# Kernel tuning notes

Measured on AMD Instinct MI355X. Metric: run time of the kernel, lower is better.

## Reference

```python
import jax, jax.numpy as jnp
import numpy as np

TEMPERATURE = 0.1

# Constant linear map replacing the nested-loop diagonal masks:
# M[i, j, k] = 1 if i + j == k, shape (10, 10, 19).
_ii, _jj = np.meshgrid(np.arange(10), np.arange(10), indexing='ij')
_M = np.zeros((10, 10, 19), dtype=np.float32)
_M[_ii, _jj, _ii + _jj] = 1.0
DIAG_SUM = jnp.asarray(_M)


def setup_inputs() -> dict:
    key = jax.random.key(0)
    ks = jax.random.split(key, 8)
    B = 16384
    grid = jax.random.normal(ks[0], (B, 4, 28, 28), dtype=jnp.float32)
    # random one-hot program ids
    pid = jax.random.randint(ks[1], (B,), 0, 4)
    program_onehot = jax.nn.one_hot(pid, 4, dtype=jnp.float32)
    W1 = jax.random.normal(ks[2], (784, 256), dtype=jnp.float32) * 0.05
    b1 = jnp.zeros((256,), dtype=jnp.float32)
    W2 = jax.random.normal(ks[3], (256, 10), dtype=jnp.float32) * 0.05
    b2 = jnp.zeros((10,), dtype=jnp.float32)
    Wp = jax.random.normal(ks[4], (4, 16), dtype=jnp.float32) * 0.3
    bp = jnp.zeros((16,), dtype=jnp.float32)
    Wr1 = jax.random.normal(ks[5], (16, 4), dtype=jnp.float32) * 0.3
    br1 = jnp.zeros((4,), dtype=jnp.float32)
    Wr2 = jax.random.normal(ks[6], (16, 4), dtype=jnp.float32) * 0.3
    br2 = jnp.zeros((4,), dtype=jnp.float32)
    return {"grid": grid, "program_onehot": program_onehot,
            "W1": W1, "b1": b1, "W2": W2, "b2": b2,
            "Wp": Wp, "bp": bp, "Wr1": Wr1, "br1": br1,
            "Wr2": Wr2, "br2": br2}


def reference(grid, program_onehot, W1, b1, W2, b2, Wp, bp, Wr1, br1, Wr2, br2):
    B = grid.shape[0]
    # digit_net: 784 -> 256 -> 10 MLP on each of the 4 sub-images
    x = grid.reshape(B * 4, 784)
    h1 = jax.nn.relu(x @ W1 + b1)
    logits = h1 @ W2 + b2                       # (B*4, 10)
    digit_probs = jax.nn.softmax(logits / TEMPERATURE, axis=-1).reshape(B, 4, 10)
    # pointer network
    h = program_onehot @ Wp + bp                 # (B, 16)
    ptr1 = jax.nn.softmax(h @ Wr1 + br1, axis=-1)  # (B, 4)
    ptr2 = jax.nn.softmax(h @ Wr2 + br2, axis=-1)  # (B, 4)
    dist1 = jnp.einsum('bp,bpd->bd', ptr1, digit_probs)  # (B, 10)
    dist2 = jnp.einsum('bp,bpd->bd', ptr2, digit_probs)  # (B, 10)
    outer = dist1[:, :, None] * dist2[:, None, :]         # (B, 10, 10)
    outer_sym = 0.5 * (outer + jnp.swapaxes(outer, 1, 2))
    # diagonal-sum convolution as one contraction against the constant map
    sum_distribution = jnp.einsum('bij,ijk->bk', outer_sym, DIAG_SUM)  # (B, 19)
    return jnp.log(sum_distribution + 1e-10)
```

## Files before the change

### kernel.cpp

```cpp
#include <hip/hip_runtime.h>
#include <hip/hip_bf16.h>

typedef __attribute__((ext_vector_type(8))) short bf16x8;
typedef __attribute__((ext_vector_type(4))) float f32x4;

__device__ __forceinline__ short f2bf(float f) {
    union { float f; unsigned u; } v; v.f = f;
    unsigned r = v.u + 0x7fffu + ((v.u >> 16) & 1u);
    return (short)(r >> 16);
}

#define KP  800
#define LDK 40
#define NKT 25

__global__ __launch_bounds__(256) void init_kernel(
    const float* __restrict__ W1, const float* __restrict__ W2,
    const float* __restrict__ Wp, const float* __restrict__ bp,
    const float* __restrict__ Wr1, const float* __restrict__ br1,
    const float* __restrict__ Wr2, const float* __restrict__ br2,
    short* __restrict__ w1t, short* __restrict__ w2t,
    float* __restrict__ ptabs)
{
    const int b = blockIdx.x;
    if (b < 200) {
        const int kt = b >> 3, nt = b & 7;
        __shared__ float tile[32][33];
        const int x = threadIdx.x & 31, y = threadIdx.x >> 5;
        #pragma unroll
        for (int r = 0; r < 4; ++r) {
            int kl = y + r * 8;
            int k = kt * 32 + kl, n = nt * 32 + x;
            tile[kl][x] = (k < 784) ? W1[k * 256 + n] : 0.f;
        }
        __syncthreads();
        #pragma unroll
        for (int r = 0; r < 4; ++r) {
            int nl = y + r * 8;
            int n = nt * 32 + nl, k = kt * 32 + x;
            w1t[n * KP + k] = f2bf(tile[x][nl]);
        }
    } else {
        for (int i = threadIdx.x; i < 16 * 256; i += 256) {
            int n = i >> 8, k = i & 255;
            float v = (n < 10) ? W2[k * 10 + n] : 0.f;
            w2t[i] = f2bf(v);
        }
        if (threadIdx.x < 8) {
            int which = threadIdx.x >> 2, p = threadIdx.x & 3;
            const float* Wr = which ? Wr2 : Wr1;
            const float* br = which ? br2 : br1;
            float s[4];
            for (int q = 0; q < 4; q++) {
                float a = br[q];
                for (int j = 0; j < 16; j++) a += (Wp[p * 16 + j] + bp[j]) * Wr[j * 4 + q];
                s[q] = a;
            }
            float m = fmaxf(fmaxf(s[0], s[1]), fmaxf(s[2], s[3]));
            float e[4]; float tot = 0.f;
            for (int q = 0; q < 4; q++) { e[q] = __expf(s[q] - m); tot += e[q]; }
            for (int q = 0; q < 4; q++) ptabs[which * 16 + p * 4 + q] = e[q] / tot;
        }
    }
}

__global__ __launch_bounds__(512, 4) void fused_kernel(
    const float* __restrict__ g_in, const float* __restrict__ onehot,
    const float* __restrict__ b1g, const float* __restrict__ b2g,
    const short* __restrict__ w1t, const short* __restrict__ w2t,
    const float* __restrict__ ptabs, float* __restrict__ out)
{
    __shared__ __align__(16) char lds[78464];
    short* Abuf = (short*)lds;
    short* Bbuf = (short*)(lds + 20480);
    short* h1   = (short*)lds;
    float* probs = (float*)(lds + 67584);
    float* dist1 = (float*)(lds + 75776);
    float* dist2 = (float*)(lds + 77056);

    const int t = threadIdx.x;
    const int lane = t & 63, wave = t >> 6;
    const int l16 = lane & 15, lg = lane >> 4;
    const int wr = wave >> 2, wc = wave & 3;
    const int blk = blockIdx.x;

    const int ar = t >> 2, aq = t & 3;
    const int bn = t >> 1, bh = t & 1;
    const float* gA = g_in + ((long)blk * 128 + ar) * 784 + aq * 8;
    const short* gB = w1t + bn * KP + bh * 16;
    short* awp = Abuf + ar * LDK + aq * 8;
    short* bwp = Bbuf + bn * LDK + bh * 16;

    f32x4 acc[4][4];
    #pragma unroll
    for (int mi = 0; mi < 4; mi++)
        #pragma unroll
        for (int ni = 0; ni < 4; ni++)
            acc[mi][ni] = (f32x4)0.f;

    f32x4 x0, x1; bf16x8 y0, y1;
    auto load_tile = [&](int kt) {
        const int k0 = kt * 32;
        if (k0 + aq * 8 < 784) {
            x0 = *(const f32x4*)(gA + k0);
            x1 = *(const f32x4*)(gA + k0 + 4);
        } else { x0 = (f32x4)0.f; x1 = (f32x4)0.f; }
        y0 = *(const bf16x8*)(gB + k0);
        y1 = *(const bf16x8*)(gB + k0 + 8);
    };
    auto write_tile = [&](int buf) {
        bf16x8 a8;
        a8[0] = f2bf(x0[0]); a8[1] = f2bf(x0[1]); a8[2] = f2bf(x0[2]); a8[3] = f2bf(x0[3]);
        a8[4] = f2bf(x1[0]); a8[5] = f2bf(x1[1]); a8[6] = f2bf(x1[2]); a8[7] = f2bf(x1[3]);
        *(bf16x8*)(awp + buf * (128 * LDK)) = a8;
        *(bf16x8*)(bwp + buf * (256 * LDK)) = y0;
        *(bf16x8*)(bwp + buf * (256 * LDK) + 8) = y1;
    };

    load_tile(0); write_tile(0);
    __syncthreads();
    int cur = 0;
    for (int kt = 0; kt < NKT; kt++) {
        const bool more = (kt + 1 < NKT);
        if (more) load_tile(kt + 1);
        const short* ab = Abuf + cur * (128 * LDK);
        const short* bb = Bbuf + cur * (256 * LDK);
        bf16x8 aF[4], bF[4];
        #pragma unroll
        for (int mi = 0; mi < 4; mi++)
            aF[mi] = *(const bf16x8*)(ab + (wr * 64 + mi * 16 + l16) * LDK + lg * 8);
        #pragma unroll
        for (int ni = 0; ni < 4; ni++)
            bF[ni] = *(const bf16x8*)(bb + (wc * 64 + ni * 16 + l16) * LDK + lg * 8);
        #pragma unroll
        for (int mi = 0; mi < 4; mi++)
            #pragma unroll
            for (int ni = 0; ni < 4; ni++)
                acc[mi][ni] = __builtin_amdgcn_mfma_f32_16x16x32_bf16(aF[mi], bF[ni], acc[mi][ni], 0, 0, 0);
        if (more) write_tile(cur ^ 1);
        __syncthreads();
        cur ^= 1;
    }

    #pragma unroll
    for (int mi = 0; mi < 4; mi++) {
        const int R = wr * 64 + mi * 16 + lg * 4;
        #pragma unroll
        for (int ni = 0; ni < 4; ni++) {
            const int N = wc * 64 + ni * 16 + l16;
            const float bias = b1g[N];
            #pragma unroll
            for (int j = 0; j < 4; j++) {
                float v = acc[mi][ni][j] + bias;
                h1[(R + j) * 264 + N] = f2bf(fmaxf(v, 0.f));
            }
        }
    }
    __syncthreads();

    f32x4 acc2 = (f32x4)0.f;
    const short* h1r = h1 + (wave * 16 + l16) * 264 + lg * 8;
    const short* w2r = w2t + l16 * 256 + lg * 8;
    #pragma unroll
    for (int kk = 0; kk < 8; kk++) {
        bf16x8 a2 = *(const bf16x8*)(h1r + kk * 32);
        bf16x8 b2f = *(const bf16x8*)(w2r + kk * 32);
        acc2 = __builtin_amdgcn_mfma_f32_16x16x32_bf16(a2, b2f, acc2, 0, 0, 0);
    }

    const float b2v = (l16 < 10) ? b2g[l16] : 0.f;
    float pv[4], mx[4];
    #pragma unroll
    for (int j = 0; j < 4; j++) {
        pv[j] = (l16 < 10) ? (acc2[j] + b2v) * 10.f : -1e30f;
        mx[j] = pv[j];
    }
    #pragma unroll
    for (int off = 1; off < 16; off <<= 1)
        #pragma unroll
        for (int j = 0; j < 4; j++)
            mx[j] = fmaxf(mx[j], __shfl_xor(mx[j], off));
    float ex[4], sm[4];
    #pragma unroll
    for (int j = 0; j < 4; j++) { ex[j] = __expf(pv[j] - mx[j]); sm[j] = ex[j]; }
    #pragma unroll
    for (int off = 1; off < 16; off <<= 1)
        #pragma unroll
        for (int j = 0; j < 4; j++)
            sm[j] += __shfl_xor(sm[j], off);
    #pragma unroll
    for (int j = 0; j < 4; j++)
        probs[(wave * 16 + lg * 4 + j) * 16 + l16] = ex[j] / sm[j];
    __syncthreads();

    if (t < 320) {
        int s = t / 10, d = t - s * 10;
        const float* oh = onehot + ((long)blk * 32 + s) * 4;
        int pid = (int)(oh[1] + 2.f * oh[2] + 3.f * oh[3] + 0.5f);
        const float* p1t = ptabs + pid * 4;
        const float* p2t = ptabs + 16 + pid * 4;
        float d1 = 0.f, d2 = 0.f;
        #pragma unroll
        for (int p = 0; p < 4; p++) {
            float pr = probs[(s * 4 + p) * 16 + d];
            d1 += p1t[p] * pr;
            d2 += p2t[p] * pr;
        }
        dist1[s * 10 + d] = d1;
        dist2[s * 10 + d] = d2;
    }
    __syncthreads();

    for (int idx = t; idx < 608; idx += 512) {
        int s = idx / 19, k = idx - s * 19;
        int ilo = k > 9 ? k - 9 : 0;
        int ihi = k < 9 ? k : 9;
        float sum = 0.f;
        for (int i = ilo; i <= ihi; i++)
            sum += dist1[s * 10 + i] * dist2[s * 10 + (k - i)];
        out[((long)blk * 32 + s) * 19 + k] = __logf(sum + 1e-10f);
    }
}

extern "C" void kernel_launch(void* const* d_in, const int* in_sizes, int n_in,
                              void* d_out, int out_size, void* d_ws, size_t ws_size,
                              hipStream_t stream)
{
    const float* grid   = (const float*)d_in[0];
    const float* onehot = (const float*)d_in[1];
    const float* W1  = (const float*)d_in[2];
    const float* b1  = (const float*)d_in[3];
    const float* W2  = (const float*)d_in[4];
    const float* b2  = (const float*)d_in[5];
    const float* Wp  = (const float*)d_in[6];
    const float* bp  = (const float*)d_in[7];
    const float* Wr1 = (const float*)d_in[8];
    const float* br1 = (const float*)d_in[9];
    const float* Wr2 = (const float*)d_in[10];
    const float* br2 = (const float*)d_in[11];
    float* out = (float*)d_out;

    short* w1t = (short*)d_ws;
    short* w2t = w1t + 256 * KP;
    float* ptabs = (float*)(w2t + 16 * 256);

    init_kernel<<<201, 256, 0, stream>>>(W1, W2, Wp, bp, Wr1, br1, Wr2, br2, w1t, w2t, ptabs);

    const int B = in_sizes[1] / 4;
    const int nblk = (B * 4) / 128;
    fused_kernel<<<nblk, 512, 0, stream>>>(grid, onehot, b1, b2, w1t, w2t, ptabs, out);
}
```

Before: 56.20 us.

## Stream W1 tiles directly to LDS with swizzle and triple-buffered pipeline

Loads the bf16 W1 tiles with global_load_lds straight into a triple-buffered, XOR-swizzled LDS layout instead of staging them through registers, and restructures the K loop into a two-step unrolled pipeline with explicit vmcnt/lgkmcnt waits and raw barriers. This is meant to cut register pressure and VGPR-to-LDS store traffic and to overlap more global loads with MFMA work. It relies on hand-placed waitcnt values and scheduling barriers, so correctness depends on the exact count of in-flight loads.

```diff
diff --git a/kernel.cpp b/kernel.cpp
--- a/kernel.cpp
+++ b/kernel.cpp
@@ -10,9 +10,24 @@
     return (short)(r >> 16);
 }
 
+__device__ __forceinline__ void gl2lds16(const void* g, void* l) {
+    __builtin_amdgcn_global_load_lds(
+        (const __attribute__((address_space(1))) unsigned int*)g,
+        (__attribute__((address_space(3))) unsigned int*)l,
+        16, 0, 0);
+}
+
 #define KP  800
 #define LDK 40
-#define NKT 25
+#define ABS (128 * LDK)
+#define BBS (256 * 32)
+#define BBSB 16384
+
+#define WAITV2 asm volatile("s_waitcnt vmcnt(2)" ::: "memory")
+#define WAITV0 asm volatile("s_waitcnt vmcnt(0)" ::: "memory")
+#define WAITL  asm volatile("s_waitcnt lgkmcnt(0)" ::: "memory")
+#define SBAR   __builtin_amdgcn_s_barrier()
+#define SCHED0 __builtin_amdgcn_sched_barrier(0)
 
 __global__ __launch_bounds__(256) void init_kernel(
     const float* __restrict__ W1, const float* __restrict__ W2,
@@ -70,13 +85,13 @@
     const short* __restrict__ w1t, const short* __restrict__ w2t,
     const float* __restrict__ ptabs, float* __restrict__ out)
 {
-    __shared__ __align__(16) char lds[78464];
+    __shared__ __align__(16) char lds[78336];
     short* Abuf = (short*)lds;
     short* Bbuf = (short*)(lds + 20480);
     short* h1   = (short*)lds;
-    float* probs = (float*)(lds + 67584);
-    float* dist1 = (float*)(lds + 75776);
-    float* dist2 = (float*)(lds + 77056);
+    float* dist1 = (float*)(lds + 67584);
+    float* dist2 = (float*)(lds + 68864);
+    float* probs = (float*)(lds + 70144);
 
     const int t = threadIdx.x;
     const int lane = t & 63, wave = t >> 6;
@@ -85,11 +100,12 @@
     const int blk = blockIdx.x;
 
     const int ar = t >> 2, aq = t & 3;
-    const int bn = t >> 1, bh = t & 1;
     const float* gA = g_in + ((long)blk * 128 + ar) * 784 + aq * 8;
-    const short* gB = w1t + bn * KP + bh * 16;
     short* awp = Abuf + ar * LDK + aq * 8;
-    short* bwp = Bbuf + bn * LDK + bh * 16;
+    const int brow = t >> 2;
+    const short* gBsw = w1t + brow * KP + ((aq ^ (brow & 3)) * 8);
+    char* ldsB = (char*)Bbuf;
+    const int bswz = lg ^ (l16 & 3);
 
     f32x4 acc[4][4];
     #pragma unroll
@@ -98,49 +114,62 @@
         for (int ni = 0; ni < 4; ni++)
             acc[mi][ni] = (f32x4)0.f;
 
-    f32x4 x0, x1; bf16x8 y0, y1;
-    auto load_tile = [&](int kt) {
+    f32x4 xa0, xa1, xb0, xb1;
+
+    auto issueB = [&](int s) {
+        const short* g0 = gBsw + s * 32;
+        char* l0 = ldsB + (s % 3) * BBSB + wave * 1024;
+        gl2lds16(g0, l0);
+        gl2lds16(g0 + 128 * KP, l0 + 8192);
+    };
+    auto issueA = [&](int kt, f32x4& x0, f32x4& x1) {
         const int k0 = kt * 32;
         if (k0 + aq * 8 < 784) {
             x0 = *(const f32x4*)(gA + k0);
             x1 = *(const f32x4*)(gA + k0 + 4);
         } else { x0 = (f32x4)0.f; x1 = (f32x4)0.f; }
-        y0 = *(const bf16x8*)(gB + k0);
-        y1 = *(const bf16x8*)(gB + k0 + 8);
-    };
-    auto write_tile = [&](int buf) {
+    };
+    auto writeA = [&](const f32x4& x0, const f32x4& x1, int buf) {
         bf16x8 a8;
         a8[0] = f2bf(x0[0]); a8[1] = f2bf(x0[1]); a8[2] = f2bf(x0[2]); a8[3] = f2bf(x0[3]);
         a8[4] = f2bf(x1[0]); a8[5] = f2bf(x1[1]); a8[6] = f2bf(x1[2]); a8[7] = f2bf(x1[3]);
-        *(bf16x8*)(awp + buf * (128 * LDK)) = a8;
-        *(bf16x8*)(bwp + buf * (256 * LDK)) = y0;
-        *(bf16x8*)(bwp + buf * (256 * LDK) + 8) = y1;
-    };
-
-    load_tile(0); write_tile(0);
-    __syncthreads();
-    int cur = 0;
-    for (int kt = 0; kt < NKT; kt++) {
-        const bool more = (kt + 1 < NKT);
-        if (more) load_tile(kt + 1);
-        const short* ab = Abuf + cur * (128 * LDK);
-        const short* bb = Bbuf + cur * (256 * LDK);
+        *(bf16x8*)(awp + buf * ABS) = a8;
+    };
+    auto mfmaStep = [&](int abuf, int bbuf) {
+        const short* ab = Abuf + abuf * ABS;
+        const short* bb = Bbuf + bbuf * BBS;
         bf16x8 aF[4], bF[4];
         #pragma unroll
         for (int mi = 0; mi < 4; mi++)
             aF[mi] = *(const bf16x8*)(ab + (wr * 64 + mi * 16 + l16) * LDK + lg * 8);
         #pragma unroll
         for (int ni = 0; ni < 4; ni++)
-            bF[ni] = *(const bf16x8*)(bb + (wc * 64 + ni * 16 + l16) * LDK + lg * 8);
+            bF[ni] = *(const bf16x8*)(bb + (wc * 64 + ni * 16 + l16) * 32 + bswz * 8);
         #pragma unroll
         for (int mi = 0; mi < 4; mi++)
             #pragma unroll
             for (int ni = 0; ni < 4; ni++)
                 acc[mi][ni] = __builtin_amdgcn_mfma_f32_16x16x32_bf16(aF[mi], bF[ni], acc[mi][ni], 0, 0, 0);
-        if (more) write_tile(cur ^ 1);
-        __syncthreads();
-        cur ^= 1;
-    }
+    };
+
+    issueB(0); SCHED0;
+    issueA(0, xa0, xa1); SCHED0;
+    writeA(xa0, xa1, 0);
+    WAITV0; WAITL; SBAR;
+
+    for (int g = 0; g < 12; ++g) {
+        const int kt = 2 * g;
+        issueB(kt + 1); issueB(kt + 2); SCHED0;
+        issueA(kt + 1, xa0, xa1); issueA(kt + 2, xb0, xb1); SCHED0;
+        mfmaStep(0, kt % 3);
+        writeA(xa0, xa1, 1);
+        WAITV2; WAITL; SBAR; SCHED0;
+        mfmaStep(1, (kt + 1) % 3);
+        writeA(xb0, xb1, 0);
+        WAITV0; WAITL; SBAR; SCHED0;
+    }
+    mfmaStep(0, 0);
+    WAITL; SBAR;
 
     #pragma unroll
     for (int mi = 0; mi < 4; mi++) {
```

Measured after the change: 56.01 us. No clear change (-0.3%).
